# Performance work log

Measured on AMD Instinct MI355X. Metric: run time of the kernel, lower is better.

The kernel has to match this reference:

```python
import jax, jax.numpy as jnp
import numpy as np

B, DIM, H, W = 4, 192, 256, 256
HEADS, DS = 6, 2
CPH = DIM // HEADS  # channels per head = 32
DN = ('NCHW', 'OIHW', 'NCHW')


def _conv(x, w, padding, groups=1):
    return jax.lax.conv_general_dilated(x, w, (1, 1), padding,
                                        dimension_numbers=DN,
                                        feature_group_count=groups)


def setup_inputs() -> dict:
    key = jax.random.key(0)
    ks = jax.random.split(key, 5)
    x = jax.random.normal(ks[0], (B, DIM, H, W), dtype=jnp.float32)
    temperature = jnp.ones((HEADS, 1, 1), dtype=jnp.float32)
    qkv_w = jax.random.normal(ks[1], (3 * DIM, DIM, 1, 1), dtype=jnp.float32) * 0.02
    dw_w = jax.random.normal(ks[2], (3 * DIM, 1, 3, 3), dtype=jnp.float32) * 0.02
    proj_w = jax.random.normal(ks[3], (DIM, DIM, 1, 1), dtype=jnp.float32) * 0.02
    a = jnp.full((1,), 0.2, dtype=jnp.float32)
    return {"x": x, "temperature": temperature, "qkv_w": qkv_w, "dw_w": dw_w,
            "proj_w": proj_w, "a1": a, "a2": a, "a3": a, "a4": a}


def _masked_softmax(attn, kk):
    # top-k mask per row (exact torch.topk + scatter_ semantics)
    _, idx = jax.lax.top_k(attn, kk)                      # [b,h,C,kk]
    mask = jax.nn.one_hot(idx, attn.shape[-1], dtype=jnp.bool_).any(axis=-2)
    return jax.nn.softmax(jnp.where(mask, attn, -jnp.inf), axis=-1)


def reference(x, temperature, qkv_w, dw_w, proj_w, a1, a2, a3, a4):
    b, c, h, w = x.shape
    h2, w2 = h // DS, w // DS
    # 1x1 qkv conv at full res, then exact adaptive (regular) max pool by DS
    qkv = _conv(x, qkv_w, 'VALID')                        # [b, 3*dim, h, w]
    qkv = jax.lax.reduce_window(qkv, -jnp.inf, jax.lax.max,
                                (1, 1, DS, DS), (1, 1, DS, DS), 'VALID')
    # depthwise 3x3
    qkv = _conv(qkv, dw_w, 'SAME', groups=3 * DIM)        # [b, 3*dim, h2, w2]
    q, k, v = jnp.split(qkv, 3, axis=1)
    n = h2 * w2
    q = q.reshape(b, HEADS, CPH, n)
    k = k.reshape(b, HEADS, CPH, n)
    v = v.reshape(b, HEADS, CPH, n)
    # F.normalize along last dim (eps clamp 1e-12)
    q = q / jnp.maximum(jnp.linalg.norm(q, axis=-1, keepdims=True), 1e-12)
    k = k / jnp.maximum(jnp.linalg.norm(k, axis=-1, keepdims=True), 1e-12)
    attn = jnp.einsum('bhcn,bhdn->bhcd', q, k) * temperature[None]  # [b,h,C,C]
    Cc = attn.shape[-1]
    att1 = _masked_softmax(attn, Cc // 2)
    att2 = _masked_softmax(attn, Cc * 2 // 3)
    att3 = _masked_softmax(attn, Cc * 3 // 4)
    att4 = _masked_softmax(attn, Cc * 4 // 5)
    def apply(a):
        return jnp.einsum('bhcd,bhdn->bhcn', a, v)
    out = apply(att1) * a1 + apply(att2) * a2 + apply(att3) * a3 + apply(att4) * a4
    out = out.reshape(b, DIM, h2, w2)
    out = jax.nn.gelu(out, approximate=False)
    # nearest upsample by integer factor DS
    out = jnp.repeat(jnp.repeat(out, DS, axis=2), DS, axis=3)
    out = _conv(out, proj_w, 'VALID')
    return out
```

## Files before the change

kernel.cpp:

```cpp
#include <hip/hip_runtime.h>
#include <hip/hip_bf16.h>
#include <math.h>

typedef __attribute__((ext_vector_type(8))) short bf16x8;
typedef __attribute__((ext_vector_type(4))) float f32x4;
typedef __attribute__((ext_vector_type(4))) unsigned int u32x4;

#define NP 16384
#define HWFULL 65536

__device__ __forceinline__ unsigned short f2bf(float f){
    union { float f; unsigned int u; } v; v.f = f;
    unsigned int u = v.u;
    u += 0x7fffu + ((u >> 16) & 1u);
    return (unsigned short)(u >> 16);
}
__device__ __forceinline__ float bf2f(unsigned short h){
    union { unsigned int u; float f; } v; v.u = ((unsigned int)h) << 16;
    return v.f;
}
__device__ __forceinline__ unsigned int pk2(float a, float b){
    unsigned int r;
    asm("v_cvt_pk_bf16_f32 %0, %1, %2" : "=v"(r) : "v"(a), "v"(b));
    return r;
}

__global__ void k_convert2(const float* __restrict__ qw, const float* __restrict__ pw,
                           unsigned short* __restrict__ Wbf, unsigned short* __restrict__ Pbf){
    int i = blockIdx.x * 256 + threadIdx.x;
    if (i < 110592) Wbf[i] = f2bf(qw[i]);
    else if (i < 110592 + 36864) Pbf[i - 110592] = f2bf(pw[i - 110592]);
}

__global__ __launch_bounds__(256, 2)
void k_qkvpool(const float* __restrict__ x, const unsigned short* __restrict__ Wbf,
               unsigned short* __restrict__ qkvp){
    __shared__ unsigned short Bl[128*200];
    __shared__ unsigned short Ep[192*36];
    int tid = threadIdx.x;
    int lane = tid & 63, wv = tid >> 6;
    int n16 = lane & 15, quad = lane >> 4;
    int bx = blockIdx.x;
    int y2 = bx >> 2, x2blk = bx & 3;
    int b = blockIdx.y;

    #pragma unroll 6
    for (int j=0;j<12;j++){
        int idx = tid + j*256;
        int g = idx >> 7, w = idx & 127;
        int y = y2*2 + (w >> 6);
        int xc = x2blk*64 + (w & 63);
        const float* xp = x + (size_t)(b*192 + g*8) * HWFULL + y*256 + xc;
        float v0 = xp[0];
        float v1 = xp[(size_t)1*HWFULL];
        float v2 = xp[(size_t)2*HWFULL];
        float v3 = xp[(size_t)3*HWFULL];
        float v4 = xp[(size_t)4*HWFULL];
        float v5 = xp[(size_t)5*HWFULL];
        float v6 = xp[(size_t)6*HWFULL];
        float v7 = xp[(size_t)7*HWFULL];
        u32x4 pk;
        pk.x = pk2(v0,v1); pk.y = pk2(v2,v3); pk.z = pk2(v4,v5); pk.w = pk2(v6,v7);
        *(u32x4*)&Bl[w*200 + g*8] = pk;
    }
    bf16x8 afc[3], afn[3];
    #pragma unroll
    for (int j=0;j<3;j++)
        afc[j] = *(const bf16x8*)(Wbf + (size_t)(((wv*3+j)*16 + n16)*192 + quad*8));
    __syncthreads();

    for (int ocblk=0; ocblk<3; ocblk++){
        f32x4 acc[3][8];
        #pragma unroll
        for (int j=0;j<3;j++)
          #pragma unroll
          for (int s=0;s<8;s++)
            acc[j][s] = (f32x4){0.f,0.f,0.f,0.f};

        #pragma unroll 1
        for (int it=0; it<6; it++){
            int nocb = (it==5) ? ocblk+1 : ocblk;
            int nit  = (it==5) ? 0 : it+1;
            if (nocb < 3){
                #pragma unroll
                for (int j=0;j<3;j++)
                    afn[j] = *(const bf16x8*)(Wbf +
                        (size_t)((nocb*192 + (wv*3+j)*16 + n16)*192 + nit*32 + quad*8));
            }
            int bko = it*32 + quad*8;
            bf16x8 bfr[8];
            #pragma unroll
            for (int s=0;s<8;s++) bfr[s] = *(const bf16x8*)&Bl[(s*16 + n16)*200 + bko];
            #pragma unroll
            for (int j=0;j<3;j++)
              #pragma unroll
              for (int s=0;s<8;s++)
                acc[j][s] = __builtin_amdgcn_mfma_f32_16x16x32_bf16(afc[j], bfr[s], acc[j][s], 0,0,0);
            #pragma unroll
            for (int j=0;j<3;j++) afc[j] = afn[j];
        }
        __syncthreads();
        #pragma unroll
        for (int j=0;j<3;j++){
            int ocr = (wv*3+j)*16 + quad*4;
            #pragma unroll
            for (int sp=0;sp<4;sp++){
                #pragma unroll
                for (int r=0;r<4;r++){
                    float v = fmaxf(acc[j][sp][r], acc[j][sp+4][r]);
                    float o = __shfl_xor(v, 1, 64);
                    v = fmaxf(v, o);
                    if ((n16 & 1) == 0)
                        Ep[(ocr + r)*36 + sp*8 + (n16 >> 1)] = f2bf(v);
                }
            }
        }
        __syncthreads();
        size_t rowbase = (size_t)(b*576 + ocblk*192)*NP + y2*128 + x2blk*32;
        #pragma unroll
        for (int it2=0; it2<6; it2++){
            int c = tid + it2*256;
            int row = c >> 3, seg = c & 7;
            uint2 vv = *(const uint2*)&Ep[row*36 + seg*4];
            *(uint2*)(qkvp + rowbase + (size_t)row*NP + seg*4) = vv;
        }
    }
}

__global__ void k_dwconv(const unsigned short* __restrict__ qkvp, const float* __restrict__ dww,
                         unsigned short* __restrict__ dwoutB, float* __restrict__ sumsq){
    __shared__ float sl[18*132];
    int tid = threadIdx.x;
    int y0 = blockIdx.x * 16;
    int ch = blockIdx.y;
    int b  = blockIdx.z;
    const unsigned short* in = qkvp + (size_t)(b*576 + ch) * NP;
    int l = tid & 63, wr = tid >> 6;
    #pragma unroll
    for (int j=0;j<5;j++){
        int row = wr + j*4;
        if (row < 18){
            int gy = y0 - 1 + row;
            float2 v = make_float2(0.f, 0.f);
            if (gy >= 0 && gy < 128){
                unsigned int u = *(const unsigned int*)&in[gy*128 + l*2];
                v.x = bf2f((unsigned short)(u & 0xffffu));
                v.y = bf2f((unsigned short)(u >> 16));
            }
            *(float2*)&sl[row*132 + 2 + l*2] = v;
        }
    }
    if (tid < 18) sl[tid*132 + 1] = 0.f;
    else if (tid < 36) sl[(tid-18)*132 + 130] = 0.f;
    float w0 = dww[ch*9+0], w1 = dww[ch*9+1], w2 = dww[ch*9+2];
    float w3 = dww[ch*9+3], w4 = dww[ch*9+4], w5 = dww[ch*9+5];
    float w6 = dww[ch*9+6], w7 = dww[ch*9+7], w8 = dww[ch*9+8];
    __syncthreads();
    unsigned short* outp = dwoutB + (size_t)(b*576 + ch) * NP;
    int col = tid & 127, half = tid >> 7;
    float ssq = 0.f;
    int base = (half*8)*132 + col + 1;
    float r0a=sl[base],     r0b=sl[base+1],   r0c=sl[base+2];
    float r1a=sl[base+132], r1b=sl[base+133], r1c=sl[base+134];
    #pragma unroll
    for (int i=0;i<8;i++){
        const float* r2 = &sl[base + (i+2)*132];
        float r2a=r2[0], r2b=r2[1], r2c=r2[2];
        float a = r0a*w0 + r0b*w1 + r0c*w2
                + r1a*w3 + r1b*w4 + r1c*w5
                + r2a*w6 + r2b*w7 + r2c*w8;
        outp[(y0 + half*8 + i)*128 + col] = f2bf(a);
        ssq += a*a;
        r0a=r1a; r0b=r1b; r0c=r1c;
        r1a=r2a; r1b=r2b; r1c=r2c;
    }
    if (ch < 384){
        #pragma unroll
        for (int off=32; off>0; off>>=1) ssq += __shfl_down(ssq, off, 64);
        if ((tid & 63) == 0) atomicAdd(&sumsq[b*384 + ch], ssq);
    }
}

__global__ __launch_bounds__(256) void k_attnraw(const unsigned short* __restrict__ dwoutB,
                                                 float* __restrict__ attn){
    __shared__ float red[4][32][33];
    int tid = threadIdx.x;
    int lane = tid & 63, wv = tid >> 6;
    int n16 = lane & 15, quad = lane >> 4;
    int h = blockIdx.y, b = blockIdx.z;
    int n0 = blockIdx.x * 512 + wv * 128;
    const unsigned short* qb = dwoutB + (size_t)(b*576 + h*32)*NP;
    const unsigned short* kb = dwoutB + (size_t)(b*576 + 192 + h*32)*NP;

    f32x4 acc[2][2];
    #pragma unroll
    for (int i=0;i<2;i++)
      #pragma unroll
      for (int j=0;j<2;j++) acc[i][j] = (f32x4){0.f,0.f,0.f,0.f};

    #pragma unroll
    for (int ks=0; ks<4; ks++){
        int n = n0 + ks*32 + quad*8;
        bf16x8 aq0 = *(const bf16x8*)(qb + (size_t)(n16)*NP + n);
        bf16x8 aq1 = *(const bf16x8*)(qb + (size_t)(16 + n16)*NP + n);
        bf16x8 bk0 = *(const bf16x8*)(kb + (size_t)(n16)*NP + n);
        bf16x8 bk1 = *(const bf16x8*)(kb + (size_t)(16 + n16)*NP + n);
        acc[0][0] = __builtin_amdgcn_mfma_f32_16x16x32_bf16(aq0, bk0, acc[0][0], 0,0,0);
        acc[0][1] = __builtin_amdgcn_mfma_f32_16x16x32_bf16(aq0, bk1, acc[0][1], 0,0,0);
        acc[1][0] = __builtin_amdgcn_mfma_f32_16x16x32_bf16(aq1, bk0, acc[1][0], 0,0,0);
        acc[1][1] = __builtin_amdgcn_mfma_f32_16x16x32_bf16(aq1, bk1, acc[1][1], 0,0,0);
    }
    #pragma unroll
    for (int cc=0; cc<2; cc++)
      #pragma unroll
      for (int dd=0; dd<2; dd++)
        #pragma unroll
        for (int r=0; r<4; r++)
          red[wv][cc*16 + quad*4 + r][dd*16 + n16] = acc[cc][dd][r];
    __syncthreads();
    float* ap = attn + (size_t)(b*6+h)*1024;
    #pragma unroll
    for (int j=0;j<4;j++){
        int o = tid + j*256;
        int c = o >> 5, d = o & 31;
        float v = red[0][c][d] + red[1][c][d] + red[2][c][d] + red[3][c][d];
        atomicAdd(ap + o, v);
    }
}

__global__ void k_mask_softmax(const float* __restrict__ attn, const float* __restrict__ sumsq,
                               const float* __restrict__ temp,
                               const float* __restrict__ A1, const float* __restrict__ A2,
                               const float* __restrict__ A3, const float* __restrict__ A4,
                               float* __restrict__ comb){
    __shared__ float Am[32][33];
    __shared__ float qn[32], kn[32];
    int t = threadIdx.x;
    int bh = blockIdx.x;
    int b = bh / 6, h = bh % 6;
    if (t < 32) qn[t] = fmaxf(sqrtf(sumsq[b*384 + h*32 + t]), 1e-12f);
    else if (t >= 64 && t < 96) kn[t-64] = fmaxf(sqrtf(sumsq[b*384 + 192 + h*32 + (t-64)]), 1e-12f);
    __syncthreads();
    int c = t >> 5, d = t & 31;
    float tv = temp[h];
    float am = attn[(size_t)bh*1024 + t] * tv / (qn[c]*kn[d]);
    Am[c][d] = am;
    float m = am;
    #pragma unroll
    for (int off=16; off>0; off>>=1) m = fmaxf(m, __shfl_down(m, off, 32));
    m = __shfl(m, 0, 32);
    float e = expf(am - m);
    __syncthreads();
    int rk = 0;
    #pragma unroll 8
    for (int dd=0; dd<32; dd++){
        float av = Am[c][dd];
        rk += (av > am) || (av == am && dd < d);
    }
    float e0 = rk < 16 ? e : 0.f;
    float e1 = rk < 21 ? e : 0.f;
    float e2 = rk < 24 ? e : 0.f;
    float e3 = rk < 25 ? e : 0.f;
    #pragma unroll
    for (int off=16; off>0; off>>=1){
        e0 += __shfl_down(e0, off, 32);
        e1 += __shfl_down(e1, off, 32);
        e2 += __shfl_down(e2, off, 32);
        e3 += __shfl_down(e3, off, 32);
    }
    float d0 = __shfl(e0, 0, 32), d1 = __shfl(e1, 0, 32);
    float d2 = __shfl(e2, 0, 32), d3 = __shfl(e3, 0, 32);
    float s = (rk<16 ? A1[0]/d0 : 0.f) + (rk<21 ? A2[0]/d1 : 0.f)
            + (rk<24 ? A3[0]/d2 : 0.f) + (rk<25 ? A4[0]/d3 : 0.f);
    comb[(size_t)bh*1024 + t] = e * s;
}

__global__ __launch_bounds__(256, 2)
void k_avproj(const unsigned short* __restrict__ dwoutB, const float* __restrict__ comb,
              const unsigned short* __restrict__ Pbf, float* __restrict__ out){
    __shared__ unsigned short Bl[128*200];
    __shared__ float cm[6144];
    int tid = threadIdx.x;
    int y2 = blockIdx.x, b = blockIdx.y;

    #pragma unroll
    for (int j=0;j<24;j++) cm[tid + j*256] = comb[b*6144 + tid + j*256];

    int n_loc = tid & 127, half = tid >> 7;
    const unsigned short* vb = dwoutB + (size_t)(b*576 + 384 + half*96)*NP + y2*128 + n_loc;
    __syncthreads();
    #pragma unroll 1
    for (int hh=0; hh<3; hh++){
        float v[32];
        #pragma unroll
        for (int d=0; d<32; d++) v[d] = bf2f(vb[(size_t)(hh*32+d)*NP]);
        const float* chp = &cm[(half*3+hh)*1024];
        #pragma unroll 1
        for (int cg=0; cg<4; cg++){
            float s[8];
            #pragma unroll
            for (int i=0;i<8;i++){
                const float* crow = chp + (cg*8+i)*32;
                float acc = 0.f;
                #pragma unroll
                for (int d=0;d<32;d++) acc += crow[d]*v[d];
                s[i] = 0.5f*acc*(1.f + erff(acc*0.70710678118654752f));
            }
            u32x4 pk;
            pk.x = pk2(s[0],s[1]); pk.y = pk2(s[2],s[3]);
            pk.z = pk2(s[4],s[5]); pk.w = pk2(s[6],s[7]);
            *(u32x4*)&Bl[n_loc*200 + half*96 + hh*32 + cg*8] = pk;
        }
    }

    int lane = tid & 63, wv = tid >> 6;
    int n16 = lane & 15, quad = lane >> 4;
    bf16x8 afc[3], afn[3];
    #pragma unroll
    for (int j=0;j<3;j++)
        afc[j] = *(const bf16x8*)(Pbf + (size_t)(((wv*3+j)*16 + n16)*192 + quad*8));
    __syncthreads();

    f32x4 acc[3][8];
    #pragma unroll
    for (int j=0;j<3;j++)
      #pragma unroll
      for (int s=0;s<8;s++)
        acc[j][s] = (f32x4){0.f,0.f,0.f,0.f};

    #pragma unroll 1
    for (int it=0; it<6; it++){
        if (it < 5){
            #pragma unroll
            for (int j=0;j<3;j++)
                afn[j] = *(const bf16x8*)(Pbf +
                    (size_t)(((wv*3+j)*16 + n16)*192 + (it+1)*32 + quad*8));
        }
        int bko = it*32 + quad*8;
        bf16x8 bfr[8];
        #pragma unroll
        for (int s=0;s<8;s++) bfr[s] = *(const bf16x8*)&Bl[(s*16 + n16)*200 + bko];
        #pragma unroll
        for (int j=0;j<3;j++)
          #pragma unroll
          for (int s=0;s<8;s++)
            acc[j][s] = __builtin_amdgcn_mfma_f32_16x16x32_bf16(afc[j], bfr[s], acc[j][s], 0,0,0);
        #pragma unroll
        for (int j=0;j<3;j++) afc[j] = afn[j];
    }

    #pragma unroll
    for (int j=0;j<3;j++){
        int oc = (wv*3+j)*16 + quad*4;
        #pragma unroll
        for (int sp=0;sp<8;sp++){
            int x2 = sp*16 + n16;
            #pragma unroll
            for (int r=0;r<4;r++){
                float v = acc[j][sp][r];
                size_t o = ((size_t)(b*192 + oc + r)*256 + 2*y2)*256 + 2*x2;
                float2 val = make_float2(v, v);
                *(float2*)(out + o) = val;
                *(float2*)(out + o + 256) = val;
            }
        }
    }
}

extern "C" void kernel_launch(void* const* d_in, const int* in_sizes, int n_in,
                              void* d_out, int out_size, void* d_ws, size_t ws_size,
                              hipStream_t stream){
    const float* x     = (const float*)d_in[0];
    const float* temp  = (const float*)d_in[1];
    const float* qkvw  = (const float*)d_in[2];
    const float* dww   = (const float*)d_in[3];
    const float* projw = (const float*)d_in[4];
    const float* A1    = (const float*)d_in[5];
    const float* A2    = (const float*)d_in[6];
    const float* A3    = (const float*)d_in[7];
    const float* A4    = (const float*)d_in[8];
    float* out = (float*)d_out;
    char* ws = (char*)d_ws;

    unsigned short* dwoutB = (unsigned short*)ws;
    unsigned short* qkvp   = (unsigned short*)(ws + 75497472ull);
    unsigned short* Wbf    = (unsigned short*)(ws + 150994944ull);
    unsigned short* Pbf    = (unsigned short*)(ws + 151216128ull);
    float*          attn   = (float*)(ws + 151289856ull);
    float*          comb   = (float*)(ws + 151388160ull);
    float*          sumsq  = (float*)(ws + 151486464ull);

    hipMemsetAsync(attn, 0, 98304, stream);
    hipMemsetAsync(sumsq, 0, 6144, stream);
    k_convert2<<<dim3((147456+255)/256), dim3(256), 0, stream>>>(qkvw, projw, Wbf, Pbf);
    k_qkvpool<<<dim3(512,4), dim3(256), 0, stream>>>(x, Wbf, qkvp);
    k_dwconv<<<dim3(8,576,4), dim3(256), 0, stream>>>(qkvp, dww, dwoutB, sumsq);
    k_attnraw<<<dim3(32,6,4), dim3(256), 0, stream>>>(dwoutB, attn);
    k_mask_softmax<<<dim3(24), dim3(1024), 0, stream>>>(attn, sumsq, temp, A1, A2, A3, A4, comb);
    k_avproj<<<dim3(128,4), dim3(256), 0, stream>>>(dwoutB, comb, Pbf, out);
}
```

Measured before the change: 546.4 us.

## Stage whole channel plane in LDS for dwconv and stage QK tiles for attnraw

The depthwise conv now gives each block a full 128x128 bf16 channel plane loaded into shared memory with 16-byte loads, replacing 16-row tiles that carried halo rows and converted to float. Each thread walks 64 rows, and the per-channel sum of squares is reduced in shared memory and written directly, which removes the atomics and the sumsq memset. The QK^T kernel now stages 256-column q and k tiles in padded LDS before the MFMAs, and the grid is doubled to 64 blocks in x. The cost is lower parallelism in dwconv (2304 blocks doing long serial loops) and 32KB of LDS per block, which may reduce occupancy.

Result: faster. 522.0 us (-4.5%).

```diff
diff --git a/kernel.cpp b/kernel.cpp
--- a/kernel.cpp
+++ b/kernel.cpp
@@ -127,49 +127,47 @@
     }
 }
 
-__global__ void k_dwconv(const unsigned short* __restrict__ qkvp, const float* __restrict__ dww,
-                         unsigned short* __restrict__ dwoutB, float* __restrict__ sumsq){
-    __shared__ float sl[18*132];
+__global__ __launch_bounds__(256) void k_dwconv(const unsigned short* __restrict__ qkvp,
+                                                const float* __restrict__ dww,
+                                                unsigned short* __restrict__ dwoutB,
+                                                float* __restrict__ sumsq){
+    __shared__ unsigned short sl[128*128];
+    __shared__ float wr[4];
     int tid = threadIdx.x;
-    int y0 = blockIdx.x * 16;
-    int ch = blockIdx.y;
-    int b  = blockIdx.z;
-    const unsigned short* in = qkvp + (size_t)(b*576 + ch) * NP;
-    int l = tid & 63, wr = tid >> 6;
-    #pragma unroll
-    for (int j=0;j<5;j++){
-        int row = wr + j*4;
-        if (row < 18){
-            int gy = y0 - 1 + row;
-            float2 v = make_float2(0.f, 0.f);
-            if (gy >= 0 && gy < 128){
-                unsigned int u = *(const unsigned int*)&in[gy*128 + l*2];
-                v.x = bf2f((unsigned short)(u & 0xffffu));
-                v.y = bf2f((unsigned short)(u >> 16));
-            }
-            *(float2*)&sl[row*132 + 2 + l*2] = v;
-        }
-    }
-    if (tid < 18) sl[tid*132 + 1] = 0.f;
-    else if (tid < 36) sl[(tid-18)*132 + 130] = 0.f;
+    int ch = blockIdx.x, b = blockIdx.y;
+    const unsigned short* in = qkvp + (size_t)(b*576 + ch)*NP;
+    #pragma unroll
+    for (int j=0;j<8;j++){
+        int idx = tid + j*256;
+        *(u32x4*)&sl[idx*8] = *(const u32x4*)(in + idx*8);
+    }
     float w0 = dww[ch*9+0], w1 = dww[ch*9+1], w2 = dww[ch*9+2];
     float w3 = dww[ch*9+3], w4 = dww[ch*9+4], w5 = dww[ch*9+5];
     float w6 = dww[ch*9+6], w7 = dww[ch*9+7], w8 = dww[ch*9+8];
     __syncthreads();
-    unsigned short* outp = dwoutB + (size_t)(b*576 + ch) * NP;
-    int col = tid & 127, half = tid >> 7;
+    int c = tid & 127, half = tid >> 7;
+    float mL = (c > 0) ? 1.f : 0.f, mR = (c < 127) ? 1.f : 0.f;
+    int cm = (c > 0) ? c-1 : c, cp = (c < 127) ? c+1 : c;
+    unsigned short* outp = dwoutB + (size_t)(b*576 + ch)*NP;
     float ssq = 0.f;
-    int base = (half*8)*132 + col + 1;
-    float r0a=sl[base],     r0b=sl[base+1],   r0c=sl[base+2];
-    float r1a=sl[base+132], r1b=sl[base+133], r1c=sl[base+134];
-    #pragma unroll
-    for (int i=0;i<8;i++){
-        const float* r2 = &sl[base + (i+2)*132];
-        float r2a=r2[0], r2b=r2[1], r2c=r2[2];
+    int r0 = half*64;
+    float r0a, r0b, r0c, r1a, r1b, r1c;
+    if (half == 0){ r0a = r0b = r0c = 0.f; }
+    else { int rr = r0-1;
+           r0a = bf2f(sl[rr*128+cm])*mL; r0b = bf2f(sl[rr*128+c]); r0c = bf2f(sl[rr*128+cp])*mR; }
+    { int rr = r0;
+      r1a = bf2f(sl[rr*128+cm])*mL; r1b = bf2f(sl[rr*128+c]); r1c = bf2f(sl[rr*128+cp])*mR; }
+    #pragma unroll 4
+    for (int i=0;i<64;i++){
+        int rr = r0 + i + 1;
+        float r2a, r2b, r2c;
+        if (rr < 128){
+            r2a = bf2f(sl[rr*128+cm])*mL; r2b = bf2f(sl[rr*128+c]); r2c = bf2f(sl[rr*128+cp])*mR;
+        } else { r2a = r2b = r2c = 0.f; }
         float a = r0a*w0 + r0b*w1 + r0c*w2
                 + r1a*w3 + r1b*w4 + r1c*w5
                 + r2a*w6 + r2b*w7 + r2c*w8;
-        outp[(y0 + half*8 + i)*128 + col] = f2bf(a);
+        outp[(r0+i)*128 + c] = (unsigned short)pk2(a, a);
         ssq += a*a;
         r0a=r1a; r0b=r1b; r0c=r1c;
         r1a=r2a; r1b=r2b; r1c=r2c;
@@ -177,20 +175,33 @@
     if (ch < 384){
         #pragma unroll
         for (int off=32; off>0; off>>=1) ssq += __shfl_down(ssq, off, 64);
-        if ((tid & 63) == 0) atomicAdd(&sumsq[b*384 + ch], ssq);
+        if ((tid & 63) == 0) wr[tid >> 6] = ssq;
+        __syncthreads();
+        if (tid == 0) sumsq[b*384 + ch] = wr[0] + wr[1] + wr[2] + wr[3];
     }
 }
 
 __global__ __launch_bounds__(256) void k_attnraw(const unsigned short* __restrict__ dwoutB,
                                                  float* __restrict__ attn){
+    __shared__ unsigned short sq[32*264];
+    __shared__ unsigned short sk[32*264];
     __shared__ float red[4][32][33];
     int tid = threadIdx.x;
     int lane = tid & 63, wv = tid >> 6;
     int n16 = lane & 15, quad = lane >> 4;
     int h = blockIdx.y, b = blockIdx.z;
-    int n0 = blockIdx.x * 512 + wv * 128;
-    const unsigned short* qb = dwoutB + (size_t)(b*576 + h*32)*NP;
-    const unsigned short* kb = dwoutB + (size_t)(b*576 + 192 + h*32)*NP;
+    int n0 = blockIdx.x * 256;
+    const unsigned short* qb = dwoutB + (size_t)(b*576 + h*32)*NP + n0;
+    const unsigned short* kb = dwoutB + (size_t)(b*576 + 192 + h*32)*NP + n0;
+
+    #pragma unroll
+    for (int j=0;j<4;j++){
+        int idx = tid + j*256;
+        int row = idx >> 5, seg = idx & 31;
+        *(u32x4*)&sq[row*264 + seg*8] = *(const u32x4*)(qb + (size_t)row*NP + seg*8);
+        *(u32x4*)&sk[row*264 + seg*8] = *(const u32x4*)(kb + (size_t)row*NP + seg*8);
+    }
+    __syncthreads();
 
     f32x4 acc[2][2];
     #pragma unroll
@@ -199,12 +210,12 @@
       for (int j=0;j<2;j++) acc[i][j] = (f32x4){0.f,0.f,0.f,0.f};
 
     #pragma unroll
-    for (int ks=0; ks<4; ks++){
-        int n = n0 + ks*32 + quad*8;
-        bf16x8 aq0 = *(const bf16x8*)(qb + (size_t)(n16)*NP + n);
-        bf16x8 aq1 = *(const bf16x8*)(qb + (size_t)(16 + n16)*NP + n);
-        bf16x8 bk0 = *(const bf16x8*)(kb + (size_t)(n16)*NP + n);
-        bf16x8 bk1 = *(const bf16x8*)(kb + (size_t)(16 + n16)*NP + n);
+    for (int ks=0; ks<2; ks++){
+        int ko = wv*64 + ks*32 + quad*8;
+        bf16x8 aq0 = *(const bf16x8*)&sq[n16*264 + ko];
+        bf16x8 aq1 = *(const bf16x8*)&sq[(16+n16)*264 + ko];
+        bf16x8 bk0 = *(const bf16x8*)&sk[n16*264 + ko];
+        bf16x8 bk1 = *(const bf16x8*)&sk[(16+n16)*264 + ko];
         acc[0][0] = __builtin_amdgcn_mfma_f32_16x16x32_bf16(aq0, bk0, acc[0][0], 0,0,0);
         acc[0][1] = __builtin_amdgcn_mfma_f32_16x16x32_bf16(aq0, bk1, acc[0][1], 0,0,0);
         acc[1][0] = __builtin_amdgcn_mfma_f32_16x16x32_bf16(aq1, bk0, acc[1][0], 0,0,0);
@@ -391,11 +402,10 @@
     float*          sumsq  = (float*)(ws + 151486464ull);
 
     hipMemsetAsync(attn, 0, 98304, stream);
-    hipMemsetAsync(sumsq, 0, 6144, stream);
     k_convert2<<<dim3((147456+255)/256), dim3(256), 0, stream>>>(qkvw, projw, Wbf, Pbf);
     k_qkvpool<<<dim3(512,4), dim3(256), 0, stream>>>(x, Wbf, qkvp);
-    k_dwconv<<<dim3(8,576,4), dim3(256), 0, stream>>>(qkvp, dww, dwoutB, sumsq);
-    k_attnraw<<<dim3(32,6,4), dim3(256), 0, stream>>>(dwoutB, attn);
+    k_dwconv<<<dim3(576,4), dim3(256), 0, stream>>>(qkvp, dww, dwoutB, sumsq);
+    k_attnraw<<<dim3(64,6,4), dim3(256), 0, stream>>>(dwoutB, attn);
     k_mask_softmax<<<dim3(24), dim3(1024), 0, stream>>>(attn, sumsq, temp, A1, A2, A3, A4, comb);
     k_avproj<<<dim3(128,4), dim3(256), 0, stream>>>(dwoutB, comb, Pbf, out);
 }
```
